# Performance work log

Measured on AMD Instinct MI355X. Metric: run time of the kernel, lower is better.

Reference implementation:

```python
import jax, jax.numpy as jnp
import numpy as np

K = 16
NUM_RBF = 32
MAX_DIST = 24.0
OUT_DIM = 256
_SPACING = MAX_DIST / (NUM_RBF - 1)
GAMMA = 1.0 / (_SPACING * _SPACING + 1e-08)
CENTERS = jnp.linspace(0.0, MAX_DIST, NUM_RBF)


def setup_inputs() -> dict:
    key = jax.random.key(0)
    k1, k2, k3 = jax.random.split(key, 3)
    B, M = 64, 1024
    # scale coords so pairwise distances span roughly [0, MAX_DIST]
    ligand_coords = jax.random.normal(k1, (B, M, 3), dtype=jnp.float32) * 8.0
    ligand_mask = jax.random.randint(k2, (B, M), 0, 2) > 0
    proj_w = jax.random.normal(k3, (OUT_DIM, K * NUM_RBF), dtype=jnp.float32) * 0.05
    return {"ligand_coords": ligand_coords, "ligand_mask": ligand_mask, "proj_w": proj_w}


def reference(ligand_coords, ligand_mask, proj_w):
    B, M, _ = ligand_coords.shape
    x = ligand_coords.astype(jnp.float32)
    # pairwise euclidean distances via the gram trick (avoids [B,M,M,3])
    sq = jnp.sum(x * x, axis=-1)                      # [B, M]
    gram = jnp.einsum('bid,bjd->bij', x, x)           # [B, M, M]
    d2 = sq[:, :, None] + sq[:, None, :] - 2.0 * gram
    dists = jnp.sqrt(jnp.maximum(d2, 1e-12))          # [B, M, M]
    eye = jnp.eye(M, dtype=bool)[None]
    valid_pair = ligand_mask[:, :, None] & ligand_mask[:, None, :]
    invalid = eye | ~valid_pair
    dists = jnp.where(invalid, jnp.inf, dists)
    # k smallest distances per atom
    neg_topk, _ = jax.lax.top_k(-dists, K)            # [B, M, K]
    topk = -neg_topk
    d_padded = jnp.where(jnp.isfinite(topk), topk, MAX_DIST)
    # RBF embed
    diff = d_padded[..., None] - CENTERS              # [B, M, K, NUM_RBF]
    rbf = jnp.exp(-GAMMA * diff * diff)
    rbf_flat = rbf.reshape(B, M, K * NUM_RBF)
    out = jnp.einsum('bmf,of->bmo', rbf_flat, proj_w)
    return out * ligand_mask[..., None].astype(out.dtype)
```

## Files before the change

kernel.cpp:

```cpp
#include <hip/hip_runtime.h>
#include <hip/hip_bf16.h>
#include <math.h>

#define MDIM 1024
#define QTOT 65536
#define KTOP 16
#define ODIM 256
#define FDIM 512

typedef float f32x4 __attribute__((ext_vector_type(4)));
typedef short s16x8 __attribute__((ext_vector_type(8)));
typedef unsigned u32x4 __attribute__((ext_vector_type(4)));

#if __has_builtin(__builtin_amdgcn_exp2f)
#define EXP2(x) __builtin_amdgcn_exp2f(x)
#else
#define EXP2(x) exp2f(x)
#endif

#define VMIN(a,b)    ({float r_; asm("v_min_f32 %0,%1,%2":"=v"(r_):"v"(a),"v"(b)); r_;})
#define VMAX(a,b)    ({float r_; asm("v_max_f32 %0,%1,%2":"=v"(r_):"v"(a),"v"(b)); r_;})

__device__ __forceinline__ int read_mask(const void* m, int i, bool is8) {
  return is8 ? (int)((const unsigned char*)m)[i] : ((const int*)m)[i];
}

__device__ __forceinline__ unsigned pack2(float lo, float hi) {
  __hip_bfloat162 h = __float22bfloat162_rn(make_float2(lo, hi));
  unsigned u;
  __builtin_memcpy(&u, &h, sizeof(u));
  return u;
}

__global__ __launch_bounds__(256) void wconv_kernel(
    const float* __restrict__ W, u32x4* __restrict__ Wb)
{
  int slot = blockIdx.x * 256 + threadIdx.x;
  int cg = slot >> 10;
  int rem = slot & 1023;
  int s = rem >> 6, l = rem & 63;
  int col = cg * 16 + (l & 15);
  int kk = s * 32 + (l >> 4) * 8;
  const float4* p = (const float4*)(W + (size_t)col * FDIM + kk);
  float4 a = p[0], b = p[1];
  u32x4 u0;
  u0[0] = pack2(a.x, a.y); u0[1] = pack2(a.z, a.w);
  u0[2] = pack2(b.x, b.y); u0[3] = pack2(b.z, b.w);
  Wb[(size_t)(cg * 16 + s) * 64 + l] = u0;
}

__global__ __launch_bounds__(256, 8) void topk_kernel(
    const float* __restrict__ coords, const void* __restrict__ mask,
    float* __restrict__ dists)
{
  __shared__ float4 pts[MDIM];
  __shared__ short posof[MDIM];
  __shared__ int s_cnt;
  __shared__ int s_is8;
  const int tid = threadIdx.x;
  const int lane = tid & 63;
  const int wv = tid >> 6;
  const int bid = blockIdx.x;
  const int batch = bid >> 5;
  const int qchunk = bid & 31;

  if (tid == 0) { s_cnt = 0; s_is8 = 0; }
  __syncthreads();
  {
    unsigned w = ((const unsigned*)mask)[tid & 255];
    if (w > 1u) atomicOr(&s_is8, 1);
  }
  __syncthreads();
  const bool is8 = (s_is8 != 0);

  const float* cb = coords + (size_t)batch * MDIM * 3;
  const int mbase = batch * MDIM;

  #pragma unroll
  for (int r = 0; r < 4; ++r) {
    int a = r * 256 + tid;
    int v = read_mask(mask, mbase + a, is8);
    float x = cb[a*3+0], y = cb[a*3+1], z = cb[a*3+2];
    float S = fmaf(z, z, fmaf(y, y, x * x));
    unsigned long long bal = __ballot(v != 0);
    int base = 0;
    if (lane == 0) base = atomicAdd(&s_cnt, __popcll(bal));
    base = __shfl(base, 0);
    int pos = base + __popcll(bal & ((1ull << lane) - 1ull));
    if (v) {
      float4 p; p.x = x; p.y = y; p.z = z; p.w = S;
      pts[pos] = p;
    }
    posof[a] = (short)(v ? pos : -1);
  }
  __syncthreads();
  const int cnt = s_cnt;
  const int cntP = (cnt + 63) & ~63;
  for (int i = cnt + tid; i < cntP; i += 256) {
    float4 p; p.x = 0.f; p.y = 0.f; p.z = 0.f; p.w = 3.0e38f;
    pts[i] = p;
  }
  __syncthreads();

  const int qi = lane & 7;
  const int part = lane >> 3;
  const int qlocal = qchunk * 32 + wv * 8 + qi;
  const float qx = cb[qlocal*3+0], qy = cb[qlocal*3+1], qz = cb[qlocal*3+2];
  const float Q = fmaf(qz, qz, fmaf(qy, qy, qx * qx));
  const float m2x = -2.0f * qx, m2y = -2.0f * qy, m2z = -2.0f * qz;
  const int selfpos = posof[qlocal];
  const int lo = (cntP * part) >> 3;
  const int ng = cntP >> 6;

  float t[16];
  #pragma unroll
  for (int i = 0; i < 16; ++i) t[i] = 3.0e38f;

  for (int g = 0; g < ng; ++g) {
    const int base = lo + g * 8;
    float s[8];
    #pragma unroll
    for (int i = 0; i < 8; ++i) {
      int idx = base + i;
      float4 p = pts[idx];
      float d = fmaf(p.z, m2z, fmaf(p.y, m2y, fmaf(p.x, m2x, p.w)));
      s[i] = (idx == selfpos) ? 3.0e38f : d;
    }
    #define CES(i,j) { float mn_ = VMIN(s[i], s[j]); float mx_ = VMAX(s[i], s[j]); s[i] = mn_; s[j] = mx_; }
    CES(0,1) CES(2,3) CES(4,5) CES(6,7)
    CES(0,2) CES(1,3) CES(4,6) CES(5,7)
    CES(1,2) CES(5,6)
    CES(0,4) CES(1,5) CES(2,6) CES(3,7)
    CES(2,4) CES(3,5)
    CES(1,2) CES(3,4) CES(5,6)
    #undef CES
    #pragma unroll
    for (int i = 0; i < 8; ++i) t[8 + i] = VMIN(t[8 + i], s[7 - i]);
    #define CET(i,j) { float mn_ = VMIN(t[i], t[j]); float mx_ = VMAX(t[i], t[j]); t[i] = mn_; t[j] = mx_; }
    CET(0,8) CET(1,9) CET(2,10) CET(3,11) CET(4,12) CET(5,13) CET(6,14) CET(7,15)
    CET(0,4) CET(1,5) CET(2,6)  CET(3,7)  CET(8,12) CET(9,13) CET(10,14) CET(11,15)
    CET(0,2) CET(1,3) CET(4,6)  CET(5,7)  CET(8,10) CET(9,11) CET(12,14) CET(13,15)
    CET(0,1) CET(2,3) CET(4,5)  CET(6,7)  CET(8,9)  CET(10,11) CET(12,13) CET(14,15)
    #undef CET
  }

  #pragma unroll
  for (int stepi = 0; stepi < 3; ++stepi) {
    const int step = 8 << stepi;
    float o_[16], m[16];
    #pragma unroll
    for (int i = 0; i < 16; ++i) o_[i] = __shfl(t[i], lane ^ step);
    #pragma unroll
    for (int i = 0; i < 16; ++i) m[i] = VMIN(t[i], o_[15 - i]);
    #define CE(i,jj) { float a_ = VMIN(m[i], m[jj]); float b_ = VMAX(m[i], m[jj]); m[i] = a_; m[jj] = b_; }
    CE(0,8) CE(1,9) CE(2,10) CE(3,11) CE(4,12) CE(5,13) CE(6,14) CE(7,15)
    CE(0,4) CE(1,5) CE(2,6)  CE(3,7)  CE(8,12) CE(9,13) CE(10,14) CE(11,15)
    CE(0,2) CE(1,3) CE(4,6)  CE(5,7)  CE(8,10) CE(9,11) CE(12,14) CE(13,15)
    CE(0,1) CE(2,3) CE(4,5)  CE(6,7)  CE(8,9)  CE(10,11) CE(12,13) CE(14,15)
    #undef CE
    #pragma unroll
    for (int i = 0; i < 16; ++i) t[i] = m[i];
  }

  if (part == 0) {
    int mq = read_mask(mask, mbase + qlocal, is8);
    float res[16];
    #pragma unroll
    for (int i = 0; i < 16; ++i) {
      float v = t[i];
      float d = (v > 1.0e37f) ? 24.0f : sqrtf(fmaxf(v + Q, 1e-12f));
      res[i] = mq ? d : -1.0f;
    }
    float4* dst = (float4*)(dists + (size_t)(mbase + qlocal) * KTOP);
    float4 o0, o1, o2, o3;
    o0.x=res[0];  o0.y=res[1];  o0.z=res[2];  o0.w=res[3];
    o1.x=res[4];  o1.y=res[5];  o1.z=res[6];  o1.w=res[7];
    o2.x=res[8];  o2.y=res[9];  o2.z=res[10]; o2.w=res[11];
    o3.x=res[12]; o3.y=res[13]; o3.z=res[14]; o3.w=res[15];
    dst[0]=o0; dst[1]=o1; dst[2]=o2; dst[3]=o3;
  }
}

constexpr double SPd = 24.0 / 31.0;
constexpr double SP2d = SPd * SPd;
constexpr float ALPHA = (float)(-(SP2d / (SP2d + 1e-8)) * 1.4426950408889634);
constexpr float INV_SP = (float)(1.0 / SPd);

__device__ __forceinline__ void gen_cell(u32x4* Ah, int rowh, int s, float d0) {
  float d = (d0 < 0.f) ? 1.0e9f : d0;
  float u = d * INV_SP;
  float C1 = (-2.0f * ALPHA) * u;
  float C0 = ALPHA * u * u;
  #pragma unroll
  for (int c8 = 0; c8 < 4; ++c8) {
    u32x4 ch;
    #pragma unroll
    for (int q = 0; q < 4; ++q) {
      const int j0 = c8 * 8 + q * 2;
      float e0 = EXP2(fmaf(C1, (float)j0,       C0) + ALPHA * (float)(j0 * j0));
      float e1 = EXP2(fmaf(C1, (float)(j0 + 1), C0) + ALPHA * (float)((j0 + 1) * (j0 + 1)));
      ch[q] = pack2(e0, e1);
    }
    Ah[s * 65 + c8 * 16 + rowh] = ch;
  }
}

__global__ __launch_bounds__(512, 4) void rbf_gemm_kernel(
    const float* __restrict__ dists, const u32x4* __restrict__ Wb,
    float* __restrict__ out)
{
  __shared__ u32x4 A_sh[4][1040];

  const int tid = threadIdx.x;
  const int lane = tid & 63;
  const int wv = tid >> 6;
  const int qbase = blockIdx.x * 64;
  const size_t dbase = (size_t)qbase * KTOP;

  float dv0 = dists[dbase + tid];
  float dv1 = dists[dbase + 512 + tid];
  {
    const int c0 = tid, c1 = tid + 512;
    gen_cell(&A_sh[c0 >> 8][0], (c0 >> 4) & 15, c0 & 15, dv0);
    gen_cell(&A_sh[c1 >> 8][0], (c1 >> 4) & 15, c1 & 15, dv1);
  }
  __syncthreads();

  f32x4 acc[4][2];
  #pragma unroll
  for (int rf = 0; rf < 4; ++rf)
    #pragma unroll
    for (int e = 0; e < 2; ++e) acc[rf][e] = (f32x4){0.f, 0.f, 0.f, 0.f};

  u32x4 bcur[2], bnxt[2];
  #pragma unroll
  for (int e = 0; e < 2; ++e)
    bcur[e] = Wb[(size_t)((e * 8 + wv) * 16) * 64 + lane];

  #pragma unroll
  for (int s = 0; s < 16; ++s) {
    if (s < 15) {
      #pragma unroll
      for (int e = 0; e < 2; ++e)
        bnxt[e] = Wb[(size_t)((e * 8 + wv) * 16 + s + 1) * 64 + lane];
    }
    s16x8 a[4], b[2];
    #pragma unroll
    for (int rf = 0; rf < 4; ++rf) {
      u32x4 ra = A_sh[rf][s * 65 + lane];
      __builtin_memcpy(&a[rf], &ra, sizeof(ra));
    }
    #pragma unroll
    for (int e = 0; e < 2; ++e) __builtin_memcpy(&b[e], &bcur[e], sizeof(u32x4));
    #pragma unroll
    for (int rf = 0; rf < 4; ++rf)
      #pragma unroll
      for (int e = 0; e < 2; ++e)
        acc[rf][e] = __builtin_amdgcn_mfma_f32_16x16x32_bf16(a[rf], b[e], acc[rf][e], 0, 0, 0);
    #pragma unroll
    for (int e = 0; e < 2; ++e) bcur[e] = bnxt[e];
  }

  const int rb_ = (lane >> 4) * 4;
  #pragma unroll
  for (int rf = 0; rf < 4; ++rf) {
    #pragma unroll
    for (int e = 0; e < 2; ++e) {
      const int col = (e * 8 + wv) * 16 + (lane & 15);
      #pragma unroll
      for (int r = 0; r < 4; ++r)
        out[(size_t)(qbase + rf * 16 + rb_ + r) * ODIM + col] = acc[rf][e][r];
    }
  }
}

extern "C" void kernel_launch(void* const* d_in, const int* in_sizes, int n_in,
                              void* d_out, int out_size, void* d_ws, size_t ws_size,
                              hipStream_t stream) {
  const float* coords = (const float*)d_in[0];
  const void* mask = d_in[1];
  const float* W = (const float*)d_in[2];
  float* out = (float*)d_out;
  float* dists = (float*)d_ws;
  u32x4* Wb = (u32x4*)((char*)d_ws + (QTOT * KTOP * 4));

  hipLaunchKernelGGL(wconv_kernel, dim3(64), dim3(256), 0, stream, W, Wb);
  hipLaunchKernelGGL(topk_kernel, dim3(QTOT / 32), dim3(256), 0, stream,
                     coords, mask, dists);
  hipLaunchKernelGGL(rbf_gemm_kernel, dim3(QTOT / 64), dim3(512), 0, stream,
                     dists, Wb, out);
}
```

Measured before the change: 63.69 us.

## Fuse top-k distance search with RBF-projection GEMM in one kernel

After: 55.14 us. 13.4% less time.

```diff
diff --git a/kernel.cpp b/kernel.cpp
--- a/kernel.cpp
+++ b/kernel.cpp
@@ -49,14 +49,43 @@
   Wb[(size_t)(cg * 16 + s) * 64 + l] = u0;
 }
 
-__global__ __launch_bounds__(256, 8) void topk_kernel(
+constexpr double SPd = 24.0 / 31.0;
+constexpr double SP2d = SPd * SPd;
+constexpr float ALPHA = (float)(-(SP2d / (SP2d + 1e-8)) * 1.4426950408889634);
+constexpr float INV_SP = (float)(1.0 / SPd);
+
+__device__ __forceinline__ void gen_cell(u32x4* Ab, int rf, int rowlo, int s, float d0) {
+  float d = (d0 < 0.f) ? 1.0e9f : d0;
+  float u = d * INV_SP;
+  float C1 = (-2.0f * ALPHA) * u;
+  float C0 = ALPHA * u * u;
+  #pragma unroll
+  for (int c8 = 0; c8 < 4; ++c8) {
+    u32x4 ch;
+    #pragma unroll
+    for (int q = 0; q < 4; ++q) {
+      const int j0 = c8 * 8 + q * 2;
+      float e0 = EXP2(fmaf(C1, (float)j0,       C0) + ALPHA * (float)(j0 * j0));
+      float e1 = EXP2(fmaf(C1, (float)(j0 + 1), C0) + ALPHA * (float)((j0 + 1) * (j0 + 1)));
+      ch[q] = pack2(e0, e1);
+    }
+    Ab[rf * 1040 + s * 65 + c8 * 16 + rowlo] = ch;
+  }
+}
+
+__global__ __launch_bounds__(256, 4) void fused_kernel(
     const float* __restrict__ coords, const void* __restrict__ mask,
-    float* __restrict__ dists)
+    const u32x4* __restrict__ Wb, float* __restrict__ out)
 {
-  __shared__ float4 pts[MDIM];
-  __shared__ short posof[MDIM];
+  __shared__ __align__(16) char raw[33280];
+  __shared__ float dvals[32][17];
   __shared__ int s_cnt;
   __shared__ int s_is8;
+
+  float4* pts = (float4*)raw;
+  short* posof = (short*)(raw + 16384);
+  u32x4* Ab = (u32x4*)raw;
+
   const int tid = threadIdx.x;
   const int lane = tid & 63;
   const int wv = tid >> 6;
@@ -104,7 +133,8 @@
 
   const int qi = lane & 7;
   const int part = lane >> 3;
-  const int qlocal = qchunk * 32 + wv * 8 + qi;
+  const int qlo = wv * 8 + qi;
+  const int qlocal = qchunk * 32 + qlo;
   const float qx = cb[qlocal*3+0], qy = cb[qlocal*3+1], qz = cb[qlocal*3+2];
   const float Q = fmaf(qz, qz, fmaf(qy, qy, qx * qx));
   const float m2x = -2.0f * qx, m2y = -2.0f * qy, m2z = -2.0f * qz;
@@ -164,109 +194,65 @@
 
   if (part == 0) {
     int mq = read_mask(mask, mbase + qlocal, is8);
-    float res[16];
     #pragma unroll
     for (int i = 0; i < 16; ++i) {
       float v = t[i];
       float d = (v > 1.0e37f) ? 24.0f : sqrtf(fmaxf(v + Q, 1e-12f));
-      res[i] = mq ? d : -1.0f;
-    }
-    float4* dst = (float4*)(dists + (size_t)(mbase + qlocal) * KTOP);
-    float4 o0, o1, o2, o3;
-    o0.x=res[0];  o0.y=res[1];  o0.z=res[2];  o0.w=res[3];
-    o1.x=res[4];  o1.y=res[5];  o1.z=res[6];  o1.w=res[7];
-    o2.x=res[8];  o2.y=res[9];  o2.z=res[10]; o2.w=res[11];
-    o3.x=res[12]; o3.y=res[13]; o3.z=res[14]; o3.w=res[15];
-    dst[0]=o0; dst[1]=o1; dst[2]=o2; dst[3]=o3;
-  }
-}
-
-constexpr double SPd = 24.0 / 31.0;
-constexpr double SP2d = SPd * SPd;
-constexpr float ALPHA = (float)(-(SP2d / (SP2d + 1e-8)) * 1.4426950408889634);
-constexpr float INV_SP = (float)(1.0 / SPd);
-
-__device__ __forceinline__ void gen_cell(u32x4* Ah, int rowh, int s, float d0) {
-  float d = (d0 < 0.f) ? 1.0e9f : d0;
-  float u = d * INV_SP;
-  float C1 = (-2.0f * ALPHA) * u;
-  float C0 = ALPHA * u * u;
-  #pragma unroll
-  for (int c8 = 0; c8 < 4; ++c8) {
-    u32x4 ch;
-    #pragma unroll
-    for (int q = 0; q < 4; ++q) {
-      const int j0 = c8 * 8 + q * 2;
-      float e0 = EXP2(fmaf(C1, (float)j0,       C0) + ALPHA * (float)(j0 * j0));
-      float e1 = EXP2(fmaf(C1, (float)(j0 + 1), C0) + ALPHA * (float)((j0 + 1) * (j0 + 1)));
-      ch[q] = pack2(e0, e1);
-    }
-    Ah[s * 65 + c8 * 16 + rowh] = ch;
-  }
-}
-
-__global__ __launch_bounds__(512, 4) void rbf_gemm_kernel(
-    const float* __restrict__ dists, const u32x4* __restrict__ Wb,
-    float* __restrict__ out)
-{
-  __shared__ u32x4 A_sh[4][1040];
-
-  const int tid = threadIdx.x;
-  const int lane = tid & 63;
-  const int wv = tid >> 6;
-  const int qbase = blockIdx.x * 64;
-  const size_t dbase = (size_t)qbase * KTOP;
-
-  float dv0 = dists[dbase + tid];
-  float dv1 = dists[dbase + 512 + tid];
-  {
-    const int c0 = tid, c1 = tid + 512;
-    gen_cell(&A_sh[c0 >> 8][0], (c0 >> 4) & 15, c0 & 15, dv0);
-    gen_cell(&A_sh[c1 >> 8][0], (c1 >> 4) & 15, c1 & 15, dv1);
-  }
-  __syncthreads();
-
-  f32x4 acc[4][2];
-  #pragma unroll
-  for (int rf = 0; rf < 4; ++rf)
-    #pragma unroll
-    for (int e = 0; e < 2; ++e) acc[rf][e] = (f32x4){0.f, 0.f, 0.f, 0.f};
-
-  u32x4 bcur[2], bnxt[2];
-  #pragma unroll
-  for (int e = 0; e < 2; ++e)
-    bcur[e] = Wb[(size_t)((e * 8 + wv) * 16) * 64 + lane];
+      dvals[qlo][i] = mq ? d : -1.0f;
+    }
+  }
+  __syncthreads();
+
+  #pragma unroll
+  for (int i = 0; i < 2; ++i) {
+    int cellid = tid + 256 * i;
+    int row = cellid >> 4, slot = cellid & 15;
+    gen_cell(Ab, row >> 4, row & 15, slot, dvals[row][slot]);
+  }
+  __syncthreads();
+
+  f32x4 acc[2][4];
+  #pragma unroll
+  for (int rf = 0; rf < 2; ++rf)
+    #pragma unroll
+    for (int e = 0; e < 4; ++e) acc[rf][e] = (f32x4){0.f, 0.f, 0.f, 0.f};
+
+  u32x4 bcur[4], bnxt[4];
+  #pragma unroll
+  for (int e = 0; e < 4; ++e)
+    bcur[e] = Wb[(size_t)((e * 4 + wv) * 16) * 64 + lane];
 
   #pragma unroll
   for (int s = 0; s < 16; ++s) {
     if (s < 15) {
       #pragma unroll
-      for (int e = 0; e < 2; ++e)
-        bnxt[e] = Wb[(size_t)((e * 8 + wv) * 16 + s + 1) * 64 + lane];
-    }
-    s16x8 a[4], b[2];
-    #pragma unroll
-    for (int rf = 0; rf < 4; ++rf) {
-      u32x4 ra = A_sh[rf][s * 65 + lane];
+      for (int e = 0; e < 4; ++e)
+        bnxt[e] = Wb[(size_t)((e * 4 + wv) * 16 + s + 1) * 64 + lane];
+    }
+    s16x8 a[2], b[4];
+    #pragma unroll
+    for (int rf = 0; rf < 2; ++rf) {
+      u32x4 ra = Ab[rf * 1040 + s * 65 + lane];
       __builtin_memcpy(&a[rf], &ra, sizeof(ra));
     }
     #pragma unroll
-    for (int e = 0; e < 2; ++e) __builtin_memcpy(&b[e], &bcur[e], sizeof(u32x4));
-    #pragma unroll
-    for (int rf = 0; rf < 4; ++rf)
+    for (int e = 0; e < 4; ++e) __builtin_memcpy(&b[e], &bcur[e], sizeof(u32x4));
+    #pragma unroll
+    for (int rf = 0; rf < 2; ++rf)
       #pragma unroll
-      for (int e = 0; e < 2; ++e)
+      for (int e = 0; e < 4; ++e)
         acc[rf][e] = __builtin_amdgcn_mfma_f32_16x16x32_bf16(a[rf], b[e], acc[rf][e], 0, 0, 0);
     #pragma unroll
-    for (int e = 0; e < 2; ++e) bcur[e] = bnxt[e];
-  }
-
+    for (int e = 0; e < 4; ++e) bcur[e] = bnxt[e];
+  }
+
+  const int qbase = mbase + qchunk * 32;
   const int rb_ = (lane >> 4) * 4;
   #pragma unroll
-  for (int rf = 0; rf < 4; ++rf) {
-    #pragma unroll
-    for (int e = 0; e < 2; ++e) {
-      const int col = (e * 8 + wv) * 16 + (lane & 15);
+  for (int rf = 0; rf < 2; ++rf) {
+    #pragma unroll
+    for (int e = 0; e < 4; ++e) {
+      const int col = (e * 4 + wv) * 16 + (lane & 15);
       #pragma unroll
       for (int r = 0; r < 4; ++r)
         out[(size_t)(qbase + rf * 16 + rb_ + r) * ODIM + col] = acc[rf][e][r];
@@ -281,12 +267,9 @@
   const void* mask = d_in[1];
   const float* W = (const float*)d_in[2];
   float* out = (float*)d_out;
-  float* dists = (float*)d_ws;
-  u32x4* Wb = (u32x4*)((char*)d_ws + (QTOT * KTOP * 4));
+  u32x4* Wb = (u32x4*)d_ws;
 
   hipLaunchKernelGGL(wconv_kernel, dim3(64), dim3(256), 0, stream, W, Wb);
-  hipLaunchKernelGGL(topk_kernel, dim3(QTOT / 32), dim3(256), 0, stream,
-                     coords, mask, dists);
-  hipLaunchKernelGGL(rbf_gemm_kernel, dim3(QTOT / 64), dim3(512), 0, stream,
-                     dists, Wb, out);
-}
+  hipLaunchKernelGGL(fused_kernel, dim3(QTOT / 32), dim3(256), 0, stream,
+                     coords, mask, Wb, out);
+}
```
